# Kernel tuning notes

Hardware: AMD Instinct MI355X
Metric: run time of the kernel (lower is better)

The kernel has to match this reference:

```python
import jax, jax.numpy as jnp
import numpy as np

B, C, IN, OUT = 2048, 64, 512, 512


def setup_inputs() -> dict:
    key = jax.random.key(0)
    k1, k2, k3 = jax.random.split(key, 3)
    x = jax.random.normal(k1, (B, IN), dtype=jnp.float32)
    index = jax.random.randint(k2, (B,), 0, C, dtype=jnp.int64)
    # kaiming_uniform-ish init: bound = sqrt(6 / ((1 + 5) * fan_in)) = 1/sqrt(fan_in)
    bound = 1.0 / np.sqrt(IN)
    weight = jax.random.uniform(k3, (C, OUT, IN), dtype=jnp.float32,
                                minval=-bound, maxval=bound)
    return {"input": x, "index": index, "weight": weight}


def reference(input, index, weight):
    # weight: (C, OUT, IN); index: (B,); input: (B, IN)
    w = weight[index]                      # (B, OUT, IN) gathered per-sample matrix
    return jnp.einsum('boi,bi->bo', w, input)  # batched matvec -> (B, OUT)
```

## Files before the change

kernel.cpp:

```cpp
#include <hip/hip_runtime.h>


constexpr int Bsz  = 2048;
constexpr int Ccnt = 64;
constexpr int INF  = 512;
constexpr int OUTF = 512;
constexpr int THREADS = 256;
constexpr int OT = 16;
constexpr int NBLK = (Ccnt * (OUTF / OT)) / 4;

typedef __attribute__((ext_vector_type(8))) short bf16x8;
typedef __attribute__((ext_vector_type(4))) float f32x4;

#if __has_builtin(__builtin_amdgcn_cvt_pk_bf16_f32)
typedef __attribute__((ext_vector_type(2))) __bf16 bf16x2_t;
__device__ __forceinline__ int cvt2i(float a, float b) {
    union { bf16x2_t v; int i; } u;
    u.v = __builtin_amdgcn_cvt_pk_bf16_f32(a, b);
    return u.i;
}
#else
__device__ __forceinline__ unsigned f2bf(float f) {
    union { float f; unsigned u; } v; v.f = f;
    return (v.u + 0x7FFFu + ((v.u >> 16) & 1u)) >> 16;
}
__device__ __forceinline__ int cvt2i(float a, float b) {
    return (int)(f2bf(a) | (f2bf(b) << 16));
}
#endif

__device__ __forceinline__ bf16x8 cvt8(float4 a, float4 b) {
    union { bf16x8 v; int i[4]; } u;
    u.i[0] = cvt2i(a.x, a.y);
    u.i[1] = cvt2i(a.z, a.w);
    u.i[2] = cvt2i(b.x, b.y);
    u.i[3] = cvt2i(b.z, b.w);
    return u.v;
}

__global__ __launch_bounds__(THREADS, 2)
void switching_linear_kernel(const float* __restrict__ x,
                             const int* __restrict__ idx,
                             const float* __restrict__ w,
                             float* __restrict__ out) {
    __shared__ unsigned short list[Bsz];
    __shared__ int ls_n;

    const int tid  = threadIdx.x;
    const int wave = tid >> 6;
    const int lane = tid & 63;
    const int c  = blockIdx.x >> 3;
    const int o0 = ((blockIdx.x & 7) * 4 + wave) * OT;
    const int mrow = lane & 15;
    const int quad = lane >> 4;

    if (tid == 0) ls_n = 0;
    __syncthreads();

    int my[8];
#pragma unroll
    for (int i = 0; i < 8; ++i) my[i] = idx[tid + i * THREADS];

    const float* aptr = w + ((size_t)c * OUTF + (size_t)(o0 + mrow)) * INF + quad * 8;
    float4 wv[32];
#pragma unroll
    for (int t = 0; t < 16; ++t) {
        wv[2 * t]     = *(const float4*)(aptr + t * 32);
        wv[2 * t + 1] = *(const float4*)(aptr + t * 32 + 4);
    }

#pragma unroll
    for (int i = 0; i < 8; ++i)
        if (my[i] == c) list[atomicAdd(&ls_n, 1)] = (unsigned short)(tid + i * THREADS);

    __syncthreads();
    const int n = ls_n;

    bf16x8 wf[16];
#pragma unroll
    for (int t = 0; t < 16; ++t) wf[t] = cvt8(wv[2 * t], wv[2 * t + 1]);

    for (int g0 = 0; g0 < n; g0 += 16) {
        const int s = g0 + mrow;
        const bool v = (s < n);
        const float* bp = x + (size_t)(v ? (int)list[s] : 0) * INF + quad * 8;

        f32x4 acc = {0.f, 0.f, 0.f, 0.f};
#pragma unroll
        for (int t = 0; t < 16; ++t) {
            bf16x8 xf;
            if (v) {
                float4 b0 = *(const float4*)(bp + t * 32);
                float4 b1 = *(const float4*)(bp + t * 32 + 4);
                xf = cvt8(b0, b1);
            } else {
                xf = (bf16x8){0, 0, 0, 0, 0, 0, 0, 0};
            }
            acc = __builtin_amdgcn_mfma_f32_16x16x32_bf16(wf[t], xf, acc, 0, 0, 0);
        }

        if (v) {
            float* dst = out + (size_t)list[s] * OUTF + o0 + quad * 4;
            *(float4*)dst = make_float4(acc[0], acc[1], acc[2], acc[3]);
        }
    }
}

extern "C" void kernel_launch(void* const* d_in, const int* in_sizes, int n_in,
                              void* d_out, int out_size, void* d_ws, size_t ws_size,
                              hipStream_t stream) {
    const float* x   = (const float*)d_in[0];
    const int*   idx = (const int*)d_in[1];
    const float* w   = (const float*)d_in[2];
    float* out = (float*)d_out;

    switching_linear_kernel<<<dim3(NBLK), dim3(THREADS), 0, stream>>>(x, idx, w, out);
}
```

Baseline: 121.4 us.

## Split K across waves with LDS reduction and quadruple block count

Each block now covers one 16-row output tile of a single expert, and its four waves each take a quarter of the input dimension. Partial MFMA results are combined through shared memory, which cuts per-thread weight registers and allows higher occupancy (launch bounds raised to 6). Weight loads become nontemporal. The per-expert sample list is capped at 128 entries to shrink LDS use, which silently drops samples if an expert receives more than 128 rows, and each 16-sample group now costs two block-wide barriers.

```diff
diff --git a/kernel.cpp b/kernel.cpp
--- a/kernel.cpp
+++ b/kernel.cpp
@@ -7,7 +7,8 @@
 constexpr int OUTF = 512;
 constexpr int THREADS = 256;
 constexpr int OT = 16;
-constexpr int NBLK = (Ccnt * (OUTF / OT)) / 4;
+constexpr int NBLK = Ccnt * (OUTF / OT);
+constexpr int LCAP = 128;
 
 typedef __attribute__((ext_vector_type(8))) short bf16x8;
 typedef __attribute__((ext_vector_type(4))) float f32x4;
@@ -29,7 +30,7 @@
 }
 #endif
 
-__device__ __forceinline__ bf16x8 cvt8(float4 a, float4 b) {
+__device__ __forceinline__ bf16x8 cvt8(f32x4 a, f32x4 b) {
     union { bf16x8 v; int i[4]; } u;
     u.i[0] = cvt2i(a.x, a.y);
     u.i[1] = cvt2i(a.z, a.w);
@@ -38,21 +39,23 @@
     return u.v;
 }
 
-__global__ __launch_bounds__(THREADS, 2)
+__global__ __launch_bounds__(THREADS, 6)
 void switching_linear_kernel(const float* __restrict__ x,
                              const int* __restrict__ idx,
                              const float* __restrict__ w,
                              float* __restrict__ out) {
-    __shared__ unsigned short list[Bsz];
+    __shared__ unsigned short list[LCAP];
     __shared__ int ls_n;
+    __shared__ float red[3][4][64];
 
     const int tid  = threadIdx.x;
     const int wave = tid >> 6;
     const int lane = tid & 63;
-    const int c  = blockIdx.x >> 3;
-    const int o0 = ((blockIdx.x & 7) * 4 + wave) * OT;
+    const int c  = blockIdx.x >> 5;
+    const int o0 = (blockIdx.x & 31) * OT;
     const int mrow = lane & 15;
     const int quad = lane >> 4;
+    const int k0   = wave * (INF / 4);
 
     if (tid == 0) ls_n = 0;
     __syncthreads();
@@ -61,37 +64,41 @@
 #pragma unroll
     for (int i = 0; i < 8; ++i) my[i] = idx[tid + i * THREADS];
 
-    const float* aptr = w + ((size_t)c * OUTF + (size_t)(o0 + mrow)) * INF + quad * 8;
-    float4 wv[32];
+    const float* aptr = w + ((size_t)c * OUTF + (size_t)(o0 + mrow)) * INF
+                          + k0 + quad * 8;
+    f32x4 wv[8];
 #pragma unroll
-    for (int t = 0; t < 16; ++t) {
-        wv[2 * t]     = *(const float4*)(aptr + t * 32);
-        wv[2 * t + 1] = *(const float4*)(aptr + t * 32 + 4);
+    for (int t = 0; t < 4; ++t) {
+        wv[2 * t]     = __builtin_nontemporal_load((const f32x4*)(aptr + t * 32));
+        wv[2 * t + 1] = __builtin_nontemporal_load((const f32x4*)(aptr + t * 32 + 4));
     }
 
 #pragma unroll
     for (int i = 0; i < 8; ++i)
-        if (my[i] == c) list[atomicAdd(&ls_n, 1)] = (unsigned short)(tid + i * THREADS);
+        if (my[i] == c) {
+            int p = atomicAdd(&ls_n, 1);
+            if (p < LCAP) list[p] = (unsigned short)(tid + i * THREADS);
+        }
 
     __syncthreads();
-    const int n = ls_n;
+    const int n = ls_n < LCAP ? ls_n : LCAP;
 
-    bf16x8 wf[16];
+    bf16x8 wf[4];
 #pragma unroll
-    for (int t = 0; t < 16; ++t) wf[t] = cvt8(wv[2 * t], wv[2 * t + 1]);
+    for (int t = 0; t < 4; ++t) wf[t] = cvt8(wv[2 * t], wv[2 * t + 1]);
 
     for (int g0 = 0; g0 < n; g0 += 16) {
         const int s = g0 + mrow;
         const bool v = (s < n);
-        const float* bp = x + (size_t)(v ? (int)list[s] : 0) * INF + quad * 8;
+        const float* bp = x + (size_t)(v ? (int)list[s] : 0) * INF + k0 + quad * 8;
 
         f32x4 acc = {0.f, 0.f, 0.f, 0.f};
 #pragma unroll
-        for (int t = 0; t < 16; ++t) {
+        for (int t = 0; t < 4; ++t) {
             bf16x8 xf;
             if (v) {
-                float4 b0 = *(const float4*)(bp + t * 32);
-                float4 b1 = *(const float4*)(bp + t * 32 + 4);
+                f32x4 b0 = *(const f32x4*)(bp + t * 32);
+                f32x4 b1 = *(const f32x4*)(bp + t * 32 + 4);
                 xf = cvt8(b0, b1);
             } else {
                 xf = (bf16x8){0, 0, 0, 0, 0, 0, 0, 0};
@@ -99,10 +106,20 @@
             acc = __builtin_amdgcn_mfma_f32_16x16x32_bf16(wf[t], xf, acc, 0, 0, 0);
         }
 
-        if (v) {
+        if (wave != 0) {
+#pragma unroll
+            for (int j = 0; j < 4; ++j) red[wave - 1][j][lane] = acc[j];
+        }
+        __syncthreads();
+        if (wave == 0 && v) {
+#pragma unroll
+            for (int w2 = 0; w2 < 3; ++w2)
+#pragma unroll
+                for (int j = 0; j < 4; ++j) acc[j] += red[w2][j][lane];
             float* dst = out + (size_t)list[s] * OUTF + o0 + quad * 4;
-            *(float4*)dst = make_float4(acc[0], acc[1], acc[2], acc[3]);
+            *(f32x4*)dst = acc;
         }
+        __syncthreads();
     }
 }
 
```

Result: no change. 120.4 us (-0.8%).

## Split into list-build, weight bf16 pre-swizzle, and gather GEMM kernels

Applied to the files above, without the earlier changes.

The single fused kernel becomes three launches. The first builds per-class sample lists, capped at 128 entries per class. The second converts the fp32 weights into a bf16 MFMA-fragment layout through LDS using global_load_lds. The third runs the grouped matvec, loading pre-swizzled bf16 weight fragments directly. This aims to drop the per-block scan of all 2048 indices and the in-register conversion, but it adds launch overhead and an extra full write and read of the weights. The LCAP cap silently drops samples if any class has more than 128 members.

```diff
diff --git a/kernel.cpp b/kernel.cpp
--- a/kernel.cpp
+++ b/kernel.cpp
@@ -5,9 +5,7 @@
 constexpr int Ccnt = 64;
 constexpr int INF  = 512;
 constexpr int OUTF = 512;
-constexpr int THREADS = 256;
-constexpr int OT = 16;
-constexpr int NBLK = (Ccnt * (OUTF / OT)) / 4;
+constexpr int LCAP = 128;
 
 typedef __attribute__((ext_vector_type(8))) short bf16x8;
 typedef __attribute__((ext_vector_type(4))) float f32x4;
@@ -29,7 +27,7 @@
 }
 #endif
 
-__device__ __forceinline__ bf16x8 cvt8(float4 a, float4 b) {
+__device__ __forceinline__ bf16x8 cvt8(f32x4 a, f32x4 b) {
     union { bf16x8 v; int i[4]; } u;
     u.i[0] = cvt2i(a.x, a.y);
     u.i[1] = cvt2i(a.z, a.w);
@@ -38,70 +36,106 @@
     return u.v;
 }
 
-__global__ __launch_bounds__(THREADS, 2)
-void switching_linear_kernel(const float* __restrict__ x,
-                             const int* __restrict__ idx,
-                             const float* __restrict__ w,
-                             float* __restrict__ out) {
-    __shared__ unsigned short list[Bsz];
-    __shared__ int ls_n;
+__device__ __forceinline__ void gld_lds16(const float* g, float* l) {
+    __builtin_amdgcn_global_load_lds(
+        (const __attribute__((address_space(1))) float*)g,
+        (__attribute__((address_space(3))) float*)l, 16, 0, 0);
+}
 
+__global__ __launch_bounds__(256)
+void k0_lists(const int* __restrict__ idx, int* __restrict__ counts,
+              unsigned short* __restrict__ lists) {
+    __shared__ unsigned short ll[LCAP];
+    __shared__ int lc;
+    const int c = blockIdx.x, tid = threadIdx.x;
+    if (tid == 0) lc = 0;
+    __syncthreads();
+    for (int i = tid; i < Bsz; i += 256) {
+        if (idx[i] == c) {
+            int p = atomicAdd(&lc, 1);
+            if (p < LCAP) ll[p] = (unsigned short)i;
+        }
+    }
+    __syncthreads();
+    const int n = lc < LCAP ? lc : LCAP;
+    if (tid == 0) counts[c] = n;
+    for (int i = tid; i < n; i += 256) lists[c * LCAP + i] = ll[i];
+}
+
+__global__ __launch_bounds__(256, 4)
+void k1_convert(const float* __restrict__ w, unsigned short* __restrict__ wsw) {
+    __shared__ float Wl[16 * 512];
     const int tid  = threadIdx.x;
     const int wave = tid >> 6;
     const int lane = tid & 63;
-    const int c  = blockIdx.x >> 3;
-    const int o0 = ((blockIdx.x & 7) * 4 + wave) * OT;
+    const int j = blockIdx.x;
+
+    const float* wc = w + (size_t)j * (16 * INF);
+#pragma unroll
+    for (int i = 0; i < 8; ++i) {
+        const int inst = wave * 8 + i;
+        const int r = inst >> 1;
+        const int h = inst & 1;
+        const int p = r & 7;
+        const float* src = wc + (size_t)r * INF + (h * 64 + (lane ^ p)) * 4;
+        gld_lds16(src, &Wl[inst * 256]);
+    }
+    __syncthreads();
+
+    unsigned short* dst = wsw + (size_t)j * 8192;
+#pragma unroll
+    for (int i = 0; i < 4; ++i) {
+        const int slot = i * 256 + tid;
+        const int kt = slot >> 6;
+        const int L  = slot & 63;
+        const int r  = L & 15;
+        const int p  = r & 7;
+        const int g0 = kt * 8 + (L >> 4) * 2;
+        f32x4 a0 = *(const f32x4*)&Wl[r * 512 + ((g0)     ^ p) * 4];
+        f32x4 a1 = *(const f32x4*)&Wl[r * 512 + ((g0 + 1) ^ p) * 4];
+        bf16x8 v = cvt8(a0, a1);
+        *(bf16x8*)(dst + (size_t)slot * 8) = v;
+    }
+}
+
+__global__ __launch_bounds__(256, 3)
+void k2_gemm(const float* __restrict__ x, const unsigned short* __restrict__ wsw,
+             const int* __restrict__ counts, const unsigned short* __restrict__ lists,
+             float* __restrict__ out) {
+    const int tid  = threadIdx.x;
+    const int wave = tid >> 6;
+    const int lane = tid & 63;
+    const int job  = blockIdx.x * 4 + wave;
+    const int c    = job >> 5;
+    const int o0   = (job & 31) * 16;
     const int mrow = lane & 15;
     const int quad = lane >> 4;
 
-    if (tid == 0) ls_n = 0;
-    __syncthreads();
+    const int n = counts[c];
 
-    int my[8];
-#pragma unroll
-    for (int i = 0; i < 8; ++i) my[i] = idx[tid + i * THREADS];
-
-    const float* aptr = w + ((size_t)c * OUTF + (size_t)(o0 + mrow)) * INF + quad * 8;
-    float4 wv[32];
-#pragma unroll
-    for (int t = 0; t < 16; ++t) {
-        wv[2 * t]     = *(const float4*)(aptr + t * 32);
-        wv[2 * t + 1] = *(const float4*)(aptr + t * 32 + 4);
-    }
-
-#pragma unroll
-    for (int i = 0; i < 8; ++i)
-        if (my[i] == c) list[atomicAdd(&ls_n, 1)] = (unsigned short)(tid + i * THREADS);
-
-    __syncthreads();
-    const int n = ls_n;
-
+    const bf16x8* aw = (const bf16x8*)(wsw + (size_t)job * 8192);
     bf16x8 wf[16];
 #pragma unroll
-    for (int t = 0; t < 16; ++t) wf[t] = cvt8(wv[2 * t], wv[2 * t + 1]);
+    for (int kt = 0; kt < 16; ++kt) wf[kt] = aw[kt * 64 + lane];
 
     for (int g0 = 0; g0 < n; g0 += 16) {
         const int s = g0 + mrow;
         const bool v = (s < n);
-        const float* bp = x + (size_t)(v ? (int)list[s] : 0) * INF + quad * 8;
+        const int b = v ? (int)lists[c * LCAP + s] : 0;
+        const float* bp = x + (size_t)b * INF + quad * 8;
 
         f32x4 acc = {0.f, 0.f, 0.f, 0.f};
 #pragma unroll
-        for (int t = 0; t < 16; ++t) {
-            bf16x8 xf;
-            if (v) {
-                float4 b0 = *(const float4*)(bp + t * 32);
-                float4 b1 = *(const float4*)(bp + t * 32 + 4);
-                xf = cvt8(b0, b1);
-            } else {
-                xf = (bf16x8){0, 0, 0, 0, 0, 0, 0, 0};
-            }
-            acc = __builtin_amdgcn_mfma_f32_16x16x32_bf16(wf[t], xf, acc, 0, 0, 0);
+        for (int kt = 0; kt < 16; ++kt) {
+            f32x4 b0 = *(const f32x4*)(bp + kt * 32);
+            f32x4 b1 = *(const f32x4*)(bp + kt * 32 + 4);
+            bf16x8 xf = cvt8(b0, b1);
+            acc = __builtin_amdgcn_mfma_f32_16x16x32_bf16(wf[kt], xf, acc, 0, 0, 0);
         }
 
         if (v) {
-            float* dst = out + (size_t)list[s] * OUTF + o0 + quad * 4;
-            *(float4*)dst = make_float4(acc[0], acc[1], acc[2], acc[3]);
+            float* dst = out + (size_t)b * OUTF + o0 + quad * 4;
+            *(f32x4*)dst = acc;
         }
     }
 }
@@ -114,5 +148,12 @@
     const float* w   = (const float*)d_in[2];
     float* out = (float*)d_out;
 
-    switching_linear_kernel<<<dim3(NBLK), dim3(THREADS), 0, stream>>>(x, idx, w, out);
+    char* ws = (char*)d_ws;
+    int* counts            = (int*)ws;
+    unsigned short* lists  = (unsigned short*)(ws + 256);
+    unsigned short* wsw    = (unsigned short*)(ws + 32768);
+
+    k0_lists<<<dim3(Ccnt), dim3(256), 0, stream>>>(idx, counts, lists);
+    k1_convert<<<dim3(2048), dim3(256), 0, stream>>>(w, wsw);
+    k2_gemm<<<dim3(512), dim3(256), 0, stream>>>(x, wsw, counts, lists, out);
 }
```

Measured after the change: 147.7 us. +21.6%, slower.
